# Performance work log

Hardware: AMD Instinct MI355X
Metric: run time of the kernel (lower is better)

## Reference

```python
import jax, jax.numpy as jnp
import numpy as np

B, N, C, S = 2, 250000, 32, 128


def setup_inputs() -> dict:
    key = jax.random.key(0)
    k1, k2, k3, k4 = jax.random.split(key, 4)
    # unique voxel coordinates per batch (spconv requires unique active sites)
    rng = np.random.default_rng(0)
    coords = []
    for b in range(B):
        lin = rng.choice(S * S * S, size=N, replace=False)
        x = lin // (S * S)
        y = (lin // S) % S
        z = lin % S
        coords.append(np.stack([x, y, z], axis=-1))
    coordinates = jnp.asarray(np.stack(coords, axis=0), dtype=jnp.int32)  # [B,N,3]
    features = jax.random.normal(k1, (B, N, C), dtype=jnp.float32)
    wscale = 1.0 / np.sqrt(27 * C)
    W1 = jax.random.normal(k2, (3, 3, 3, C, C), dtype=jnp.float32) * wscale
    W2 = jax.random.normal(k3, (3, 3, 3, C, C), dtype=jnp.float32) * wscale
    W3 = jax.random.normal(k4, (3, 3, 3, C, C), dtype=jnp.float32) * wscale
    return {
        "features": features,
        "coordinates": coordinates,
        "spatial_shape": jnp.array([S, S, S], dtype=jnp.int32),
        "batch_size": B,
        "W1": W1,
        "W2": W2,
        "W3": W3,
    }


def reference(features, coordinates, spatial_shape, batch_size, W1, W2, W3):
    Bs = int(batch_size)
    X, Y, Z = [int(s) for s in np.asarray(spatial_shape)]
    n = coordinates.shape[1]
    M = Bs * n
    cin = features.shape[-1]
    b_idx = jnp.repeat(jnp.arange(Bs, dtype=jnp.int32), n)  # [M]
    coords = coordinates.reshape(-1, 3).astype(jnp.int32)  # [M,3]
    feat = features.reshape(-1, cin)  # [M,Cin]
    # dense hash grid: voxel -> row index in feat, -1 if inactive
    grid = jnp.full((Bs, X, Y, Z), -1, dtype=jnp.int32)
    grid = grid.at[b_idx, coords[:, 0], coords[:, 1], coords[:, 2]].set(
        jnp.arange(M, dtype=jnp.int32))

    cx, cy, cz = coords[:, 0], coords[:, 1], coords[:, 2]

    def subm_conv(f, W):
        # submanifold 3x3x3 conv: output only at active sites, gather active
        # neighbors (rulebook gather -> GEMM -> accumulate)
        cout = W.shape[-1]
        out = jnp.zeros((M, cout), dtype=f.dtype)
        for dx in range(3):
            for dy in range(3):
                for dz in range(3):
                    nx, ny, nz = cx + dx - 1, cy + dy - 1, cz + dz - 1
                    valid = ((nx >= 0) & (nx < X) & (ny >= 0) & (ny < Y)
                             & (nz >= 0) & (nz < Z))
                    idx = grid[b_idx,
                               jnp.clip(nx, 0, X - 1),
                               jnp.clip(ny, 0, Y - 1),
                               jnp.clip(nz, 0, Z - 1)]
                    idx = jnp.where(valid, idx, -1)
                    g = jnp.where((idx >= 0)[:, None],
                                  f[jnp.maximum(idx, 0)], 0.0)
                    out = out + g @ W[dx, dy, dz]
        return out

    x = jax.nn.relu(subm_conv(feat, W1))
    x = jax.nn.relu(subm_conv(x, W2))
    x = subm_conv(x, W3)
    return x.reshape(Bs, n, -1)
```

## Files before the change

### kernel.cpp

```cpp
#include <hip/hip_runtime.h>

#define SG 128
#define C 32
#define NPB 250000
#define BATCH 2
#define M (BATCH * NPB)
#define MP 500032
#define NW (MP / 64)
#define NK 27
#define NBKT 65536
#define CAP 256
#define HSZ 1024

typedef __attribute__((ext_vector_type(4))) float f32x4;
typedef __attribute__((ext_vector_type(8))) short bf16x8;

union frag_u { unsigned u[4]; bf16x8 v; };

__device__ __forceinline__ int bucket_key(int b, int x, int y, int z) {
    return (b << 15) | ((x >> 2) << 10) | ((y >> 2) << 5) | (z >> 2);
}

__device__ __forceinline__ void gl_lds16(const void* g, void* l) {
    __builtin_amdgcn_global_load_lds(
        (const __attribute__((address_space(1))) unsigned int*)g,
        (__attribute__((address_space(3))) unsigned int*)l, 16, 0, 0);
}

__global__ void hist_kernel(const int* __restrict__ coords, int* __restrict__ hist) {
    int p = blockIdx.x * blockDim.x + threadIdx.x;
    if (p >= M) return;
    int x = coords[3 * p + 0], y = coords[3 * p + 1], z = coords[3 * p + 2];
    atomicAdd(&hist[bucket_key(p >= NPB, x, y, z)], 1);
}

__global__ __launch_bounds__(256) void scan_kernel(int* __restrict__ h) {
    __shared__ int part[256];
    int t = threadIdx.x;
    int s = 0;
    for (int i = 0; i < 256; i++) s += h[t * 256 + i];
    part[t] = s;
    __syncthreads();
    if (t == 0) {
        int run = 0;
        for (int i = 0; i < 256; i++) { int v = part[i]; part[i] = run; run += v; }
    }
    __syncthreads();
    int run = part[t];
    for (int i = 0; i < 256; i++) { int v = h[t * 256 + i]; h[t * 256 + i] = run; run += v; }
}

__global__ void place_kernel(const int* __restrict__ coords, int* __restrict__ h,
                             int* __restrict__ ord, int* __restrict__ gridP) {
    int p = blockIdx.x * blockDim.x + threadIdx.x;
    if (p >= M) return;
    int x = coords[3 * p + 0], y = coords[3 * p + 1], z = coords[3 * p + 2];
    int b = (p >= NPB) ? 1 : 0;
    int j = atomicAdd(&h[bucket_key(b, x, y, z)], 1);
    ord[j] = p;
    gridP[((b * SG + x) * SG + y) * SG + z] = j;
}

__global__ __launch_bounds__(64) void build_dedup_kernel(
    const int* __restrict__ coords, const int* __restrict__ ord,
    const int* __restrict__ gridP,
    unsigned short* __restrict__ nbL, int* __restrict__ uniq, int* __restrict__ ucnt)
{
    __shared__ int hkey[HSZ];
    __shared__ int hval[HSZ];
    __shared__ int hcnt;
    const int t = threadIdx.x;
    const int w = blockIdx.x;
    for (int i = t; i < HSZ; i += 64) { hkey[i] = -2; hval[i] = -1; }
    if (t == 0) { hcnt = 1; uniq[w * CAP] = -1; }
    __syncthreads();

    const int j = w * 64 + t;
    int x = 0, y = 0, z = 0, base = 0;
    const bool real = (j < M);
    if (real) {
        int p = ord[j];
        x = coords[3 * p + 0]; y = coords[3 * p + 1]; z = coords[3 * p + 2];
        base = (p >= NPB) ? SG * SG * SG : 0;
    }
    for (int k = 0; k < NK; k++) {
        int id = -1;
        if (real) {
            int nx = x + k / 9 - 1;
            int ny = y + (k / 3) % 3 - 1;
            int nz = z + (k % 3) - 1;
            if ((unsigned)nx < SG && (unsigned)ny < SG && (unsigned)nz < SG)
                id = gridP[base + (nx * SG + ny) * SG + nz];
        }
        int slot = 0;
        if (id >= 0) {
            unsigned h = (((unsigned)id * 2654435761u) >> 20) & (HSZ - 1);
            slot = -1;
            while (slot < 0) {
                int old = atomicCAS(&hkey[h], -2, id);
                bool won = (old == -2);
                int myslot = -1;
                if (won) myslot = atomicAdd(&hcnt, 1);
                if (won) {
                    if (myslot < CAP) { hval[h] = myslot; uniq[w * CAP + myslot] = id; slot = myslot; }
                    else { hval[h] = 0; slot = 0; }
                } else if (old == id) {
                    int v = hval[h];
                    if (v >= 0) slot = v;
                } else {
                    h = (h + 1) & (HSZ - 1);
                }
            }
        }
        nbL[((size_t)w * NK + k) * 64 + (t & 15) * 4 + (t >> 4)] = (unsigned short)slot;
    }
    __syncthreads();
    if (t == 0) ucnt[w] = (hcnt < CAP) ? hcnt : CAP;
}

__global__ void prep_w_kernel(const float* __restrict__ W, unsigned short* __restrict__ wpk) {
    int id = blockIdx.x * blockDim.x + threadIdx.x;
    if (id >= NK * 2 * 64) return;
    int l = id & 63, ct = (id >> 6) & 1, k = id >> 7;
    int lrow = l & 15, kg = l >> 4;
    unsigned hw[4], lw[4];
#pragma unroll
    for (int jp = 0; jp < 4; jp++) {
        float v0 = W[k * 1024 + (kg * 8 + 2 * jp + 0) * 32 + ct * 16 + lrow];
        float v1 = W[k * 1024 + (kg * 8 + 2 * jp + 1) * 32 + ct * 16 + lrow];
        unsigned u0 = __float_as_uint(v0), u1 = __float_as_uint(v1);
        hw[jp] = (u0 >> 16) | (u1 & 0xFFFF0000u);
        float h0 = __uint_as_float(u0 & 0xFFFF0000u);
        float h1 = __uint_as_float(u1 & 0xFFFF0000u);
        lw[jp] = (__float_as_uint(v0 - h0) >> 16) | (__float_as_uint(v1 - h1) & 0xFFFF0000u);
    }
    unsigned* dh = (unsigned*)(wpk + k * 2048 + ((ct * 2 + 0) * 64 + l) * 8);
    unsigned* dl = (unsigned*)(wpk + k * 2048 + ((ct * 2 + 1) * 64 + l) * 8);
#pragma unroll
    for (int i = 0; i < 4; i++) { dh[i] = hw[i]; dl[i] = lw[i]; }
}

__device__ __forceinline__ void split1(float v, unsigned short& h, unsigned short& lo) {
    unsigned u = __float_as_uint(v);
    h = (unsigned short)(u >> 16);
    float hf = __uint_as_float(u & 0xFFFF0000u);
    lo = (unsigned short)(__float_as_uint(v - hf) >> 16);
}

__global__ void split_in_kernel(const float* __restrict__ f, const int* __restrict__ ord,
                                unsigned short* __restrict__ fpk) {
    int id = blockIdx.x * blockDim.x + threadIdx.x;
    if (id >= M * 8) return;
    int j = id >> 3, c4 = id & 7;
    int p = ord[j];
    f32x4 v = *(const f32x4*)&f[p * 32 + c4 * 4];
    ushort4 h, lo;
    split1(v[0], h.x, lo.x);
    split1(v[1], h.y, lo.y);
    split1(v[2], h.z, lo.z);
    split1(v[3], h.w, lo.w);
    *(ushort4*)&fpk[j * 64 + c4 * 4] = h;
    *(ushort4*)&fpk[j * 64 + 32 + c4 * 4] = lo;
}

template <bool RELU, bool LAST>
__global__ __launch_bounds__(256) void conv_mfma(
    const unsigned short* __restrict__ fpk,
    const unsigned short* __restrict__ nbL,
    const int* __restrict__ uniq,
    const int* __restrict__ ucnt,
    const unsigned short* __restrict__ wpk,
    const unsigned short* __restrict__ zrow,
    const int* __restrict__ ord,
    unsigned short* __restrict__ opk,
    float* __restrict__ of32)
{
    __shared__ char bufA[CAP * 128];

    const int t = threadIdx.x;
    const int l = t & 63;
    const int wv = t >> 6;
    const int lrow = l & 15, kg = l >> 4;
    const int w = blockIdx.x;
    const int wbase = w * 64;

    const int lane_r = l >> 3;
    const int lc = l & 7;
    {
        const int cnt = ucnt[w];
        char* ldsb = bufA + wv * 64 * 128;
#pragma unroll
        for (int i = 0; i < 8; i++) {
            int r = wv * 64 + i * 8 + lane_r;
            int id = (r < cnt) ? uniq[(size_t)w * CAP + r] : -1;
            const unsigned short* src = (id >= 0)
                ? fpk + (size_t)id * 64 + ((lc ^ lane_r) << 3)
                : zrow + (lc << 3);
            gl_lds16(src, ldsb + i * 1024);
        }
    }

    const int kbeg = wv * 7;
    const int ntap = (wv == 3) ? 6 : 7;
    ushort4 q[7];
#pragma unroll
    for (int i = 0; i < 7; i++) {
        int k = kbeg + i; if (k > 26) k = 26;
        q[i] = *(const ushort4*)(nbL + ((size_t)w * NK + k) * 64 + lrow * 4);
    }
    __builtin_amdgcn_sched_barrier(0);
    __syncthreads();

    f32x4 acc[4][2];
#pragma unroll
    for (int rt = 0; rt < 4; rt++)
#pragma unroll
        for (int ct = 0; ct < 2; ct++) acc[rt][ct] = (f32x4){0.f, 0.f, 0.f, 0.f};

#define LOADW(DST, K) { \
    const unsigned short* wb_ = wpk + ((K) << 11); \
    DST[0].v = *(const bf16x8*)(wb_ + ((0 * 64 + l) << 3)); \
    DST[1].v = *(const bf16x8*)(wb_ + ((1 * 64 + l) << 3)); \
    DST[2].v = *(const bf16x8*)(wb_ + ((2 * 64 + l) << 3)); \
    DST[3].v = *(const bf16x8*)(wb_ + ((3 * 64 + l) << 3)); }

#define TAP(I, WCUR, WNXT) \
    if ((I) < ntap) { \
        if ((I) + 1 < ntap) LOADW(WNXT, kbeg + (I) + 1); \
        int rows[4] = {q[I].x & 255, q[I].y & 255, q[I].z & 255, q[I].w & 255}; \
        frag_u ah[4], al[4]; \
        _Pragma("unroll") \
        for (int rt = 0; rt < 4; rt++) { \
            int r = rows[rt]; \
            const char* rb = bufA + (r << 7); \
            int sw = (r & 7) << 4; \
            ah[rt].v = *(const bf16x8*)(rb + ((kg << 4) ^ sw)); \
            al[rt].v = *(const bf16x8*)(rb + (((kg + 4) << 4) ^ sw)); \
        } \
        _Pragma("unroll") \
        for (int rt = 0; rt < 4; rt++) acc[rt][0] = __builtin_amdgcn_mfma_f32_16x16x32_bf16(ah[rt].v, WCUR[0].v, acc[rt][0], 0, 0, 0); \
        _Pragma("unroll") \
        for (int rt = 0; rt < 4; rt++) acc[rt][1] = __builtin_amdgcn_mfma_f32_16x16x32_bf16(ah[rt].v, WCUR[2].v, acc[rt][1], 0, 0, 0); \
        _Pragma("unroll") \
        for (int rt = 0; rt < 4; rt++) acc[rt][0] = __builtin_amdgcn_mfma_f32_16x16x32_bf16(ah[rt].v, WCUR[1].v, acc[rt][0], 0, 0, 0); \
        _Pragma("unroll") \
        for (int rt = 0; rt < 4; rt++) acc[rt][1] = __builtin_amdgcn_mfma_f32_16x16x32_bf16(ah[rt].v, WCUR[3].v, acc[rt][1], 0, 0, 0); \
        _Pragma("unroll") \
        for (int rt = 0; rt < 4; rt++) acc[rt][0] = __builtin_amdgcn_mfma_f32_16x16x32_bf16(al[rt].v, WCUR[0].v, acc[rt][0], 0, 0, 0); \
        _Pragma("unroll") \
        for (int rt = 0; rt < 4; rt++) acc[rt][1] = __builtin_amdgcn_mfma_f32_16x16x32_bf16(al[rt].v, WCUR[2].v, acc[rt][1], 0, 0, 0); \
    }

    frag_u wA[4], wB[4];
    LOADW(wA, kbeg);
    TAP(0, wA, wB); TAP(1, wB, wA); TAP(2, wA, wB); TAP(3, wB, wA);
    TAP(4, wA, wB); TAP(5, wB, wA); TAP(6, wA, wB);
#undef TAP
#undef LOADW

    __syncthreads();

    f32x4* dmp = (f32x4*)bufA;
#pragma unroll
    for (int rt = 0; rt < 4; rt++)
#pragma unroll
        for (int ct = 0; ct < 2; ct++)
            dmp[((wv * 8 + rt * 2 + ct) << 6) + l] = acc[rt][ct];
    __syncthreads();

    f32x4 fin[2] = {(f32x4){0.f, 0.f, 0.f, 0.f}, (f32x4){0.f, 0.f, 0.f, 0.f}};
#pragma unroll
    for (int s = 0; s < 4; s++)
#pragma unroll
        for (int ct = 0; ct < 2; ct++)
            fin[ct] += dmp[((s * 8 + wv * 2 + ct) << 6) + l];

    const int rbase = wbase + wv * 16 + 4 * kg;
#pragma unroll
    for (int j = 0; j < 4; j++) {
        int row = rbase + j;
        if (row < M) {
            int orow = LAST ? ord[row] : row;
#pragma unroll
            for (int ct = 0; ct < 2; ct++) {
                int col = ct * 16 + lrow;
                float v = fin[ct][j];
                if (RELU) v = fmaxf(v, 0.f);
                if (LAST) {
                    of32[orow * 32 + col] = v;
                } else {
                    unsigned short h, lo;
                    split1(v, h, lo);
                    opk[row * 64 + col] = h;
                    opk[row * 64 + 32 + col] = lo;
                }
            }
        }
    }
}

extern "C" void kernel_launch(void* const* d_in, const int* in_sizes, int n_in,
                              void* d_out, int out_size, void* d_ws, size_t ws_size,
                              hipStream_t stream) {
    const float* features    = (const float*)d_in[0];
    const int*   coordinates = (const int*)d_in[1];
    const float* W1 = (const float*)d_in[4];
    const float* W2 = (const float*)d_in[5];
    const float* W3 = (const float*)d_in[6];

    char* ws = (char*)d_ws;
    const size_t GRID_BYTES = (size_t)BATCH * SG * SG * SG * 4;
    const size_t NBL_BYTES  = (size_t)NW * NK * 64 * 2;
    const size_t UNIQ_BYTES = (size_t)NW * CAP * 4;
    const size_t UCNT_BYTES = (size_t)NW * 4;
    const size_t HIST_BYTES = (size_t)NBKT * 4;
    const size_t ORD_BYTES  = (size_t)MP * 4;
    const size_t WPK_BYTES  = (size_t)NK * 2048 * 2;
    const size_t Z_BYTES    = 256;

    size_t off = 0;
    int* gridP = (int*)(ws + off); off += GRID_BYTES;
    unsigned short* nbL = (unsigned short*)(ws + off); off += NBL_BYTES;
    int* uniq  = (int*)(ws + off); off += UNIQ_BYTES;
    int* ucnt  = (int*)(ws + off); off += UCNT_BYTES;
    int* hist  = (int*)(ws + off); off += HIST_BYTES;
    int* ord   = (int*)(ws + off); off += ORD_BYTES;
    unsigned short* wpk1 = (unsigned short*)(ws + off); off += WPK_BYTES;
    unsigned short* wpk2 = (unsigned short*)(ws + off); off += WPK_BYTES;
    unsigned short* wpk3 = (unsigned short*)(ws + off); off += WPK_BYTES;
    unsigned short* zrow = (unsigned short*)(ws + off); off += Z_BYTES;
    unsigned short* fpk_a = (unsigned short*)(ws + off); off += (size_t)MP * 64 * 2;
    unsigned short* fpk_b = (unsigned short*)d_out;
    float* out = (float*)d_out;

    hipMemsetAsync(gridP, 0xFF, GRID_BYTES, stream);
    hipMemsetAsync(hist, 0, HIST_BYTES, stream);
    hipMemsetAsync(zrow, 0, Z_BYTES, stream);

    hist_kernel<<<(M + 255) / 256, 256, 0, stream>>>(coordinates, hist);
    scan_kernel<<<1, 256, 0, stream>>>(hist);
    place_kernel<<<(M + 255) / 256, 256, 0, stream>>>(coordinates, hist, ord, gridP);
    build_dedup_kernel<<<NW, 64, 0, stream>>>(coordinates, ord, gridP, nbL, uniq, ucnt);

    const int PW = NK * 2 * 64;
    prep_w_kernel<<<(PW + 255) / 256, 256, 0, stream>>>(W1, wpk1);
    prep_w_kernel<<<(PW + 255) / 256, 256, 0, stream>>>(W2, wpk2);
    prep_w_kernel<<<(PW + 255) / 256, 256, 0, stream>>>(W3, wpk3);

    split_in_kernel<<<(M * 8 + 255) / 256, 256, 0, stream>>>(features, ord, fpk_a);

    conv_mfma<true,  false><<<NW, 256, 0, stream>>>(fpk_a, nbL, uniq, ucnt, wpk1, zrow, ord, fpk_b, nullptr);
    conv_mfma<true,  false><<<NW, 256, 0, stream>>>(fpk_b, nbL, uniq, ucnt, wpk2, zrow, ord, fpk_a, nullptr);
    conv_mfma<false, true ><<<NW, 256, 0, stream>>>(fpk_a, nbL, uniq, ucnt, wpk3, zrow, ord, nullptr, out);
}
```

Measured before the change: 417.9 us.

## Parallelize histogram scan, fuse feature split into placement, shrink neighbor table

Replaces the single-block serial scan over the 65536-bucket histogram with a three-kernel parallel block scan. The bf16 hi/lo feature split moves into the placement kernel, which removes one launch and the indirect reads through ord. The three weight-prep launches become one, neighbor slot indices shrink from 16-bit to 8-bit, and the LDS dedup hash table is halved. Fusing the split into placement gives each thread strided 128-byte row reads and writes instead of coalesced ones. The 8-bit slots still hold every index, since slots never exceed 255.

```diff
diff --git a/kernel.cpp b/kernel.cpp
--- a/kernel.cpp
+++ b/kernel.cpp
@@ -10,7 +10,7 @@
 #define NK 27
 #define NBKT 65536
 #define CAP 256
-#define HSZ 1024
+#define HSZ 512
 
 typedef __attribute__((ext_vector_type(4))) float f32x4;
 typedef __attribute__((ext_vector_type(8))) short bf16x8;
@@ -25,6 +25,13 @@
     __builtin_amdgcn_global_load_lds(
         (const __attribute__((address_space(1))) unsigned int*)g,
         (__attribute__((address_space(3))) unsigned int*)l, 16, 0, 0);
+}
+
+__device__ __forceinline__ void split1(float v, unsigned short& h, unsigned short& lo) {
+    unsigned u = __float_as_uint(v);
+    h = (unsigned short)(u >> 16);
+    float hf = __uint_as_float(u & 0xFFFF0000u);
+    lo = (unsigned short)(__float_as_uint(v - hf) >> 16);
 }
 
 __global__ void hist_kernel(const int* __restrict__ coords, int* __restrict__ hist) {
@@ -34,24 +41,42 @@
     atomicAdd(&hist[bucket_key(p >= NPB, x, y, z)], 1);
 }
 
-__global__ __launch_bounds__(256) void scan_kernel(int* __restrict__ h) {
-    __shared__ int part[256];
+__global__ __launch_bounds__(256) void scan1_kernel(int* __restrict__ h, int* __restrict__ bsum) {
+    __shared__ int s[256];
+    int t = threadIdx.x, b = blockIdx.x;
+    int v = h[b * 256 + t];
+    s[t] = v;
+    __syncthreads();
+    for (int off = 1; off < 256; off <<= 1) {
+        int x = (t >= off) ? s[t - off] : 0;
+        __syncthreads();
+        s[t] += x;
+        __syncthreads();
+    }
+    h[b * 256 + t] = s[t] - v;
+    if (t == 255) bsum[b] = s[255];
+}
+__global__ __launch_bounds__(256) void scan2_kernel(int* __restrict__ bsum) {
+    __shared__ int s[256];
     int t = threadIdx.x;
-    int s = 0;
-    for (int i = 0; i < 256; i++) s += h[t * 256 + i];
-    part[t] = s;
-    __syncthreads();
-    if (t == 0) {
-        int run = 0;
-        for (int i = 0; i < 256; i++) { int v = part[i]; part[i] = run; run += v; }
-    }
-    __syncthreads();
-    int run = part[t];
-    for (int i = 0; i < 256; i++) { int v = h[t * 256 + i]; h[t * 256 + i] = run; run += v; }
-}
-
-__global__ void place_kernel(const int* __restrict__ coords, int* __restrict__ h,
-                             int* __restrict__ ord, int* __restrict__ gridP) {
+    int v = bsum[t];
+    s[t] = v;
+    __syncthreads();
+    for (int off = 1; off < 256; off <<= 1) {
+        int x = (t >= off) ? s[t - off] : 0;
+        __syncthreads();
+        s[t] += x;
+        __syncthreads();
+    }
+    bsum[t] = s[t] - v;
+}
+__global__ __launch_bounds__(256) void scan3_kernel(int* __restrict__ h, const int* __restrict__ bsum) {
+    h[blockIdx.x * 256 + threadIdx.x] += bsum[blockIdx.x];
+}
+
+__global__ void place_kernel(const int* __restrict__ coords, const float* __restrict__ f,
+                             int* __restrict__ h, int* __restrict__ ord,
+                             int* __restrict__ gridP, unsigned short* __restrict__ fpk) {
     int p = blockIdx.x * blockDim.x + threadIdx.x;
     if (p >= M) return;
     int x = coords[3 * p + 0], y = coords[3 * p + 1], z = coords[3 * p + 2];
@@ -59,12 +84,25 @@
     int j = atomicAdd(&h[bucket_key(b, x, y, z)], 1);
     ord[j] = p;
     gridP[((b * SG + x) * SG + y) * SG + z] = j;
+    const f32x4* src = (const f32x4*)(f + (size_t)p * 32);
+    unsigned short* dst = fpk + (size_t)j * 64;
+#pragma unroll
+    for (int c4 = 0; c4 < 8; c4++) {
+        f32x4 v = src[c4];
+        ushort4 hh, lo;
+        split1(v[0], hh.x, lo.x);
+        split1(v[1], hh.y, lo.y);
+        split1(v[2], hh.z, lo.z);
+        split1(v[3], hh.w, lo.w);
+        *(ushort4*)(dst + c4 * 4) = hh;
+        *(ushort4*)(dst + 32 + c4 * 4) = lo;
+    }
 }
 
 __global__ __launch_bounds__(64) void build_dedup_kernel(
     const int* __restrict__ coords, const int* __restrict__ ord,
     const int* __restrict__ gridP,
-    unsigned short* __restrict__ nbL, int* __restrict__ uniq, int* __restrict__ ucnt)
+    unsigned char* __restrict__ nbL, int* __restrict__ uniq, int* __restrict__ ucnt)
 {
     __shared__ int hkey[HSZ];
     __shared__ int hval[HSZ];
@@ -112,16 +150,21 @@
                 }
             }
         }
-        nbL[((size_t)w * NK + k) * 64 + (t & 15) * 4 + (t >> 4)] = (unsigned short)slot;
+        nbL[((size_t)w * NK + k) * 64 + (t & 15) * 4 + (t >> 4)] = (unsigned char)slot;
     }
     __syncthreads();
     if (t == 0) ucnt[w] = (hcnt < CAP) ? hcnt : CAP;
 }
 
-__global__ void prep_w_kernel(const float* __restrict__ W, unsigned short* __restrict__ wpk) {
+__global__ void prep_w_kernel(const float* __restrict__ W1, const float* __restrict__ W2,
+                              const float* __restrict__ W3, unsigned short* __restrict__ wpk) {
     int id = blockIdx.x * blockDim.x + threadIdx.x;
-    if (id >= NK * 2 * 64) return;
-    int l = id & 63, ct = (id >> 6) & 1, k = id >> 7;
+    if (id >= 3 * NK * 2 * 64) return;
+    int which = id / (NK * 128);
+    int rid = id - which * (NK * 128);
+    const float* W = which == 0 ? W1 : which == 1 ? W2 : W3;
+    unsigned short* wout = wpk + (size_t)which * NK * 2048;
+    int l = rid & 63, ct = (rid >> 6) & 1, k = rid >> 7;
     int lrow = l & 15, kg = l >> 4;
     unsigned hw[4], lw[4];
 #pragma unroll
@@ -134,39 +177,16 @@
         float h1 = __uint_as_float(u1 & 0xFFFF0000u);
         lw[jp] = (__float_as_uint(v0 - h0) >> 16) | (__float_as_uint(v1 - h1) & 0xFFFF0000u);
     }
-    unsigned* dh = (unsigned*)(wpk + k * 2048 + ((ct * 2 + 0) * 64 + l) * 8);
-    unsigned* dl = (unsigned*)(wpk + k * 2048 + ((ct * 2 + 1) * 64 + l) * 8);
+    unsigned* dh = (unsigned*)(wout + k * 2048 + ((ct * 2 + 0) * 64 + l) * 8);
+    unsigned* dl = (unsigned*)(wout + k * 2048 + ((ct * 2 + 1) * 64 + l) * 8);
 #pragma unroll
     for (int i = 0; i < 4; i++) { dh[i] = hw[i]; dl[i] = lw[i]; }
-}
-
-__device__ __forceinline__ void split1(float v, unsigned short& h, unsigned short& lo) {
-    unsigned u = __float_as_uint(v);
-    h = (unsigned short)(u >> 16);
-    float hf = __uint_as_float(u & 0xFFFF0000u);
-    lo = (unsigned short)(__float_as_uint(v - hf) >> 16);
-}
-
-__global__ void split_in_kernel(const float* __restrict__ f, const int* __restrict__ ord,
-                                unsigned short* __restrict__ fpk) {
-    int id = blockIdx.x * blockDim.x + threadIdx.x;
-    if (id >= M * 8) return;
-    int j = id >> 3, c4 = id & 7;
-    int p = ord[j];
-    f32x4 v = *(const f32x4*)&f[p * 32 + c4 * 4];
-    ushort4 h, lo;
-    split1(v[0], h.x, lo.x);
-    split1(v[1], h.y, lo.y);
-    split1(v[2], h.z, lo.z);
-    split1(v[3], h.w, lo.w);
-    *(ushort4*)&fpk[j * 64 + c4 * 4] = h;
-    *(ushort4*)&fpk[j * 64 + 32 + c4 * 4] = lo;
 }
 
 template <bool RELU, bool LAST>
 __global__ __launch_bounds__(256) void conv_mfma(
     const unsigned short* __restrict__ fpk,
-    const unsigned short* __restrict__ nbL,
+    const unsigned char* __restrict__ nbL,
     const int* __restrict__ uniq,
     const int* __restrict__ ucnt,
     const unsigned short* __restrict__ wpk,
@@ -202,11 +222,11 @@
 
     const int kbeg = wv * 7;
     const int ntap = (wv == 3) ? 6 : 7;
-    ushort4 q[7];
+    unsigned q[7];
 #pragma unroll
     for (int i = 0; i < 7; i++) {
         int k = kbeg + i; if (k > 26) k = 26;
-        q[i] = *(const ushort4*)(nbL + ((size_t)w * NK + k) * 64 + lrow * 4);
+        q[i] = *(const unsigned*)(nbL + ((size_t)w * NK + k) * 64 + lrow * 4);
     }
     __builtin_amdgcn_sched_barrier(0);
     __syncthreads();
@@ -227,7 +247,8 @@
 #define TAP(I, WCUR, WNXT) \
     if ((I) < ntap) { \
         if ((I) + 1 < ntap) LOADW(WNXT, kbeg + (I) + 1); \
-        int rows[4] = {q[I].x & 255, q[I].y & 255, q[I].z & 255, q[I].w & 255}; \
+        int rows[4] = {(int)(q[I] & 255), (int)((q[I] >> 8) & 255), \
+                       (int)((q[I] >> 16) & 255), (int)(q[I] >> 24)}; \
         frag_u ah[4], al[4]; \
         _Pragma("unroll") \
         for (int rt = 0; rt < 4; rt++) { \
@@ -310,44 +331,45 @@
 
     char* ws = (char*)d_ws;
     const size_t GRID_BYTES = (size_t)BATCH * SG * SG * SG * 4;
-    const size_t NBL_BYTES  = (size_t)NW * NK * 64 * 2;
+    const size_t NBL_BYTES  = (size_t)NW * NK * 64;
     const size_t UNIQ_BYTES = (size_t)NW * CAP * 4;
     const size_t UCNT_BYTES = (size_t)NW * 4;
     const size_t HIST_BYTES = (size_t)NBKT * 4;
+    const size_t BSUM_BYTES = 256 * 4;
     const size_t ORD_BYTES  = (size_t)MP * 4;
     const size_t WPK_BYTES  = (size_t)NK * 2048 * 2;
     const size_t Z_BYTES    = 256;
 
     size_t off = 0;
     int* gridP = (int*)(ws + off); off += GRID_BYTES;
-    unsigned short* nbL = (unsigned short*)(ws + off); off += NBL_BYTES;
+    unsigned char* nbL = (unsigned char*)(ws + off); off += NBL_BYTES;
     int* uniq  = (int*)(ws + off); off += UNIQ_BYTES;
     int* ucnt  = (int*)(ws + off); off += UCNT_BYTES;
     int* hist  = (int*)(ws + off); off += HIST_BYTES;
+    int* bsum  = (int*)(ws + off); off += BSUM_BYTES;
     int* ord   = (int*)(ws + off); off += ORD_BYTES;
-    unsigned short* wpk1 = (unsigned short*)(ws + off); off += WPK_BYTES;
-    unsigned short* wpk2 = (unsigned short*)(ws + off); off += WPK_BYTES;
-    unsigned short* wpk3 = (unsigned short*)(ws + off); off += WPK_BYTES;
+    unsigned short* wpk = (unsigned short*)(ws + off); off += 3 * WPK_BYTES;
     unsigned short* zrow = (unsigned short*)(ws + off); off += Z_BYTES;
     unsigned short* fpk_a = (unsigned short*)(ws + off); off += (size_t)MP * 64 * 2;
     unsigned short* fpk_b = (unsigned short*)d_out;
     float* out = (float*)d_out;
+    unsigned short* wpk1 = wpk;
+    unsigned short* wpk2 = wpk + NK * 2048;
+    unsigned short* wpk3 = wpk + 2 * NK * 2048;
 
     hipMemsetAsync(gridP, 0xFF, GRID_BYTES, stream);
     hipMemsetAsync(hist, 0, HIST_BYTES, stream);
     hipMemsetAsync(zrow, 0, Z_BYTES, stream);
 
     hist_kernel<<<(M + 255) / 256, 256, 0, stream>>>(coordinates, hist);
-    scan_kernel<<<1, 256, 0, stream>>>(hist);
-    place_kernel<<<(M + 255) / 256, 256, 0, stream>>>(coordinates, hist, ord, gridP);
+    scan1_kernel<<<256, 256, 0, stream>>>(hist, bsum);
+    scan2_kernel<<<1, 256, 0, stream>>>(bsum);
+    scan3_kernel<<<256, 256, 0, stream>>>(hist, bsum);
+    place_kernel<<<(M + 255) / 256, 256, 0, stream>>>(coordinates, features, hist, ord, gridP, fpk_a);
     build_dedup_kernel<<<NW, 64, 0, stream>>>(coordinates, ord, gridP, nbL, uniq, ucnt);
 
-    const int PW = NK * 2 * 64;
-    prep_w_kernel<<<(PW + 255) / 256, 256, 0, stream>>>(W1, wpk1);
-    prep_w_kernel<<<(PW + 255) / 256, 256, 0, stream>>>(W2, wpk2);
-    prep_w_kernel<<<(PW + 255) / 256, 256, 0, stream>>>(W3, wpk3);
-
-    split_in_kernel<<<(M * 8 + 255) / 256, 256, 0, stream>>>(features, ord, fpk_a);
+    const int PW = 3 * NK * 2 * 64;
+    prep_w_kernel<<<(PW + 255) / 256, 256, 0, stream>>>(W1, W2, W3, wpk);
 
     conv_mfma<true,  false><<<NW, 256, 0, stream>>>(fpk_a, nbL, uniq, ucnt, wpk1, zrow, ord, fpk_b, nullptr);
     conv_mfma<true,  false><<<NW, 256, 0, stream>>>(fpk_b, nbL, uniq, ucnt, wpk2, zrow, ord, fpk_a, nullptr);
```

Measured after the change: 382.3 us. -8.5%, faster.
